# Kernel tuning notes

Measured on AMD Instinct MI355X. Metric: run time of the kernel, lower is better.

Reference implementation:

```python
import jax, jax.numpy as jnp
import numpy as np

B, N, HID, E, H = 4, 256, 256, 64, 4
OUT = HID // 2          # 128
D = OUT // H            # 32
AGG = H * (2 * D + 1)   # 260 = concat(mean D, attn_sum 1, max D) per head


def setup_inputs() -> dict:
    key = jax.random.key(0)
    ks = jax.random.split(key, 7)
    s = 0.05
    return {
        "h_x": jax.random.normal(ks[0], (B, N, HID), jnp.float32),
        "h_e": jax.random.normal(ks[1], (B, N, N, E), jnp.float32),
        "h_m": jnp.ones((B, N), jnp.float32),
        "W_Q": jax.random.normal(ks[2], (OUT, HID), jnp.float32) * s,
        "W_K": jax.random.normal(ks[3], (OUT, E), jnp.float32) * s,
        "W_V": jax.random.normal(ks[4], (OUT, E), jnp.float32) * s,
        "W_R": jax.random.normal(ks[5], (OUT, AGG), jnp.float32) * s,
    }


def reference(h_x, h_e, h_m, W_Q, W_K, W_V, W_R):
    # queries from node features: [B,H,N,D]
    h_q = (h_x @ W_Q.T).reshape(B, N, H, D).transpose(0, 2, 1, 3)
    # keys/values from dense pairwise edge features: [B,H,N,N,D]
    h_k = jnp.einsum('bnme,ce->bnmc', h_e, W_K).reshape(B, N, N, H, D).transpose(0, 3, 1, 2, 4)
    h_v = jnp.einsum('bnme,ce->bnmc', h_e, W_V).reshape(B, N, N, H, D).transpose(0, 3, 1, 2, 4)
    # broadcast dot: [B,H,N,N]
    scores = jnp.einsum('bhnd,bhnmd->bhnm', h_q, h_k) / np.float32(np.sqrt(D))
    # per-node mask broadcast as [B,1,N,1] (masks query rows)
    scores = jnp.where(h_m[:, None, :, None] == 0, -jnp.inf, scores)
    # NOTE: original code softmaxes over dim=1 = HEAD axis (faithful)
    attn = jax.nn.softmax(scores, axis=1)                      # [B,H,N,N]
    attn_w = attn[..., None] * h_v                             # [B,H,N,N,D]
    aggr_sum = attn_w.sum(axis=3)                              # [B,H,N,D]
    attn_sum = attn.sum(axis=3, keepdims=True) + 1e-8          # [B,H,N,1]
    aggr_mean = aggr_sum / attn_sum
    aggr_max = attn_w.max(axis=3)                              # [B,H,N,D]
    multi = jnp.concatenate([aggr_mean, attn_sum, aggr_max], axis=-1)  # [B,H,N,2D+1]
    aggr_out = multi.transpose(0, 2, 1, 3).reshape(B, N, AGG)  # [B,N,260]
    return aggr_out @ W_R.T                                    # [B,N,OUT]
```

## Files before the change

### kernel.cpp

```cpp
#include <hip/hip_runtime.h>
#include <hip/hip_bf16.h>

constexpr int Bb   = 4;
constexpr int Nn   = 256;
constexpr int HID  = 256;
constexpr int Ee   = 64;
constexpr int Hh   = 4;
constexpr int OUTc = 128;
constexpr int Dd   = 32;
constexpr int AGG  = 260;

typedef __attribute__((ext_vector_type(8))) short short8;
typedef __attribute__((ext_vector_type(4))) float floatx4;
typedef __attribute__((ext_vector_type(2))) float floatx2;

__device__ __forceinline__ unsigned pk2(float a, float b) {
    union { __hip_bfloat162 h; unsigned u; } cv;
    cv.h = __float22bfloat162_rn(float2{a, b});
    return cv.u;
}

__device__ __forceinline__ short8 pack8(floatx4 f0, floatx4 f1) {
    union { short8 s; unsigned u[4]; } r;
    r.u[0] = pk2(f0[0], f0[1]);
    r.u[1] = pk2(f0[2], f0[3]);
    r.u[2] = pk2(f1[0], f1[1]);
    r.u[3] = pk2(f1[2], f1[3]);
    return r.s;
}

__device__ __forceinline__ void gload16(const float* g, float* l) {
    __builtin_amdgcn_global_load_lds(
        (const __attribute__((address_space(1))) void*)g,
        (__attribute__((address_space(3))) void*)l, 16, 0, 0);
}

__global__ __launch_bounds__(256, 2)
void eama_fused(const float* __restrict__ h_x, const float* __restrict__ h_e,
                const float* __restrict__ h_m,
                const float* __restrict__ W_Q, const float* __restrict__ W_K,
                const float* __restrict__ W_V, const float* __restrict__ W_R,
                float* __restrict__ out)
{
    __shared__ __align__(16) float sStage[4][2][4][64][4];
    __shared__ __align__(16) float sS[4][16][4];
    __shared__ __align__(16) unsigned short sWin[256 * 8];
    __shared__ __align__(16) float sQp[256];

    const int tid  = threadIdx.x;
    const int lane = tid & 63;
    const int w    = tid >> 6;
    const int ncol = lane & 15;
    const int q8   = lane >> 4;
    const int bn   = blockIdx.x;
    const float maskv = h_m[bn];

    const float* heb = h_e + (size_t)bn * Nn * Ee;
    const float* arq = heb + (size_t)(w * 64 + ncol) * Ee + q8 * 8;

    #define STAGE(it_, buf_) do { \
        const float* ar_ = arq + (size_t)(it_) * 16 * Ee; \
        gload16(ar_,      &sStage[w][buf_][0][0][0]); \
        gload16(ar_ + 4,  &sStage[w][buf_][1][0][0]); \
        gload16(ar_ + 32, &sStage[w][buf_][2][0][0]); \
        gload16(ar_ + 36, &sStage[w][buf_][3][0][0]); \
    } while (0)

    STAGE(0, 0);
    STAGE(1, 1);

    short8 bfV[8][2];
    {
        const int ncol_e = tid & 15;
        const int q8_e   = (tid >> 4) & 3;
        const int ks_e   = (tid >> 6) & 1;
        const int cthi   = tid >> 7;
        #pragma unroll
        for (int c = 0; c < 4; ++c) {
            const int ct = c * 2 + cthi;
            const float* row = W_V + (size_t)(ct * 16 + ncol_e) * Ee + ks_e * 32 + q8_e * 8;
            short8 v = pack8(*(const floatx4*)row, *(const floatx4*)(row + 4));
            *(short8*)&sWin[tid * 8] = v;
            __syncthreads();
            #pragma unroll
            for (int m = 0; m < 4; ++m)
                bfV[c * 2 + (m >> 1)][m & 1] = *(const short8*)&sWin[(m * 64 + lane) * 8];
            __syncthreads();
        }
    }

    {
        const int c = tid & 127, half = tid >> 7;
        const float* wq = W_Q + (size_t)c * HID + half * 128;
        const float* xr = h_x + (size_t)bn * HID + half * 128;
        float acc = 0.f;
        #pragma unroll
        for (int i = 0; i < 32; ++i) {
            floatx4 a = *(const floatx4*)(wq + i * 4);
            floatx4 x = *(const floatx4*)(xr + i * 4);
            acc = fmaf(a[0], x[0], fmaf(a[1], x[1], fmaf(a[2], x[2], fmaf(a[3], x[3], acc))));
        }
        sQp[tid] = acc;
    }
    __syncthreads();
    if (tid < 128) sQp[tid] += sQp[tid + 128];
    __syncthreads();

    float* sU = &sS[0][0][0];
    {
        const int h = tid >> 6, e = tid & 63;
        float acc = 0.f;
        #pragma unroll
        for (int d = 0; d < 32; ++d)
            acc = fmaf(sQp[h * 32 + d], W_K[(size_t)(h * Dd + d) * Ee + e], acc);
        sU[h * 64 + e] = acc * 0.1767766952966369f;
    }
    __syncthreads();

    short8 bu0 = {0, 0, 0, 0, 0, 0, 0, 0};
    short8 bu1 = {0, 0, 0, 0, 0, 0, 0, 0};
    if (ncol < Hh) {
        bu0 = pack8(*(const floatx4*)&sU[ncol * 64 + q8 * 8],
                    *(const floatx4*)&sU[ncol * 64 + q8 * 8 + 4]);
        bu1 = pack8(*(const floatx4*)&sU[ncol * 64 + 32 + q8 * 8],
                    *(const floatx4*)&sU[ncol * 64 + 32 + q8 * 8 + 4]);
    }
    __syncthreads();

    float vs[8], vm[8], asumH = 0.f;
    #pragma unroll
    for (int ct = 0; ct < 8; ++ct) { vs[ct] = 0.f; vm[ct] = -3.402823466e38f; }

    #pragma unroll
    for (int it = 0; it < 4; ++it) {
        const int buf = it & 1;
        if (it < 3) asm volatile("s_waitcnt vmcnt(4)" ::: "memory");
        else        asm volatile("s_waitcnt vmcnt(0)" ::: "memory");

        floatx4 c0 = *(const floatx4*)&sStage[w][buf][0][lane][0];
        floatx4 c1 = *(const floatx4*)&sStage[w][buf][1][lane][0];
        floatx4 c2 = *(const floatx4*)&sStage[w][buf][2][lane][0];
        floatx4 c3 = *(const floatx4*)&sStage[w][buf][3][lane][0];
        short8 af0 = pack8(c0, c1);
        short8 af1 = pack8(c2, c3);
        if (it < 2) {
            asm volatile("s_waitcnt lgkmcnt(0)" ::: "memory");
            STAGE(it + 2, buf);
        }

        floatx4 accV[8], accS = (floatx4){0, 0, 0, 0};
        #pragma unroll
        for (int ct = 0; ct < 8; ++ct) accV[ct] = (floatx4){0, 0, 0, 0};
        #pragma unroll
        for (int ct = 0; ct < 8; ++ct) {
            accV[ct] = __builtin_amdgcn_mfma_f32_16x16x32_bf16(af0, bfV[ct][0], accV[ct], 0, 0, 0);
            accV[ct] = __builtin_amdgcn_mfma_f32_16x16x32_bf16(af1, bfV[ct][1], accV[ct], 0, 0, 0);
        }
        accS = __builtin_amdgcn_mfma_f32_16x16x32_bf16(af0, bu0, accS, 0, 0, 0);
        accS = __builtin_amdgcn_mfma_f32_16x16x32_bf16(af1, bu1, accS, 0, 0, 0);

        if (ncol < Hh) {
            #pragma unroll
            for (int r = 0; r < 4; ++r)
                sS[w][q8 * 4 + r][ncol] = (maskv != 0.f) ? accS[r] : -1e30f;
        }
        __builtin_amdgcn_wave_barrier();

        #pragma unroll
        for (int r = 0; r < 4; ++r) {
            floatx4 sc = *(const floatx4*)&sS[w][q8 * 4 + r][0];
            float e0 = __expf(sc[0]), e1 = __expf(sc[1]);
            float e2 = __expf(sc[2]), e3 = __expf(sc[3]);
            float inv = 1.f / ((e0 + e1) + (e2 + e3));
            float a0 = e0 * inv, a1 = e1 * inv, a2 = e2 * inv, a3 = e3 * inv;
            asumH += (ncol & 2) ? ((ncol & 1) ? a3 : a2) : ((ncol & 1) ? a1 : a0);
            float p;
            p = a0 * accV[0][r]; vs[0] += p; vm[0] = fmaxf(vm[0], p);
            p = a0 * accV[1][r]; vs[1] += p; vm[1] = fmaxf(vm[1], p);
            p = a1 * accV[2][r]; vs[2] += p; vm[2] = fmaxf(vm[2], p);
            p = a1 * accV[3][r]; vs[3] += p; vm[3] = fmaxf(vm[3], p);
            p = a2 * accV[4][r]; vs[4] += p; vm[4] = fmaxf(vm[4], p);
            p = a2 * accV[5][r]; vs[5] += p; vm[5] = fmaxf(vm[5], p);
            p = a3 * accV[6][r]; vs[6] += p; vm[6] = fmaxf(vm[6], p);
            p = a3 * accV[7][r]; vs[7] += p; vm[7] = fmaxf(vm[7], p);
        }
        __builtin_amdgcn_wave_barrier();
    }
    #undef STAGE

    #pragma unroll
    for (int ct = 0; ct < 8; ++ct) {
        vs[ct] += __shfl_xor(vs[ct], 16, 64);
        vs[ct] += __shfl_xor(vs[ct], 32, 64);
        vm[ct] = fmaxf(vm[ct], __shfl_xor(vm[ct], 16, 64));
        vm[ct] = fmaxf(vm[ct], __shfl_xor(vm[ct], 32, 64));
    }
    asumH += __shfl_xor(asumH, 16, 64);
    asumH += __shfl_xor(asumH, 32, 64);

    float* SB = &sStage[0][0][0][0][0];
    if (lane < 16) {
        #pragma unroll
        for (int ct = 0; ct < 8; ++ct) {
            SB[w * 2048 + ct * 16 + lane]       = vs[ct];
            SB[w * 2048 + 128 + ct * 16 + lane] = vm[ct];
        }
    }
    if (lane < Hh) SB[w * 2048 + 256 + lane] = asumH;
    __syncthreads();
    if (tid < Hh) {
        SB[512 + tid] = 1e-8f +
            (SB[0 * 2048 + 256 + tid] + SB[1 * 2048 + 256 + tid]) +
            (SB[2 * 2048 + 256 + tid] + SB[3 * 2048 + 256 + tid]);
    }
    __syncthreads();
    if (tid < OUTc) {
        float vsum = (SB[0 * 2048 + tid] + SB[1 * 2048 + tid]) +
                     (SB[2 * 2048 + tid] + SB[3 * 2048 + tid]);
        float vmax = fmaxf(fmaxf(SB[0 * 2048 + 128 + tid], SB[1 * 2048 + 128 + tid]),
                           fmaxf(SB[2 * 2048 + 128 + tid], SB[3 * 2048 + 128 + tid]));
        const int h = tid >> 5, d = tid & 31;
        SB[768 + h * 65 + d]      = vsum / SB[512 + h];
        SB[768 + h * 65 + 33 + d] = vmax;
        if (tid < Hh) SB[768 + tid * 65 + 32] = SB[512 + tid];
    }
    __syncthreads();
    {
        const int c = tid & 127, part = tid >> 7;
        const int j0 = part * 130;
        const float* wr = W_R + (size_t)c * AGG + j0;
        const float* sM = SB + 768;
        float a0 = 0.f, a1 = 0.f, a2 = 0.f, a3 = 0.f;
        #pragma unroll 8
        for (int j = 0; j < 128; j += 4) {
            floatx2 A  = *(const floatx2*)(wr + j);
            floatx2 Bv = *(const floatx2*)(wr + j + 2);
            a0 = fmaf(sM[j0 + j],     A[0],  a0);
            a1 = fmaf(sM[j0 + j + 1], A[1],  a1);
            a2 = fmaf(sM[j0 + j + 2], Bv[0], a2);
            a3 = fmaf(sM[j0 + j + 3], Bv[1], a3);
        }
        floatx2 T = *(const floatx2*)(wr + 128);
        a0 = fmaf(sM[j0 + 128], T[0], a0);
        a1 = fmaf(sM[j0 + 129], T[1], a1);
        SB[1100 + part * 128 + c] = (a0 + a1) + (a2 + a3);
    }
    __syncthreads();
    if (tid < OUTc)
        out[(size_t)bn * OUTc + tid] = SB[1100 + tid] + SB[1100 + 128 + tid];
}

extern "C" void kernel_launch(void* const* d_in, const int* in_sizes, int n_in,
                              void* d_out, int out_size, void* d_ws, size_t ws_size,
                              hipStream_t stream) {
    const float* h_x = (const float*)d_in[0];
    const float* h_e = (const float*)d_in[1];
    const float* h_m = (const float*)d_in[2];
    const float* W_Q = (const float*)d_in[3];
    const float* W_K = (const float*)d_in[4];
    const float* W_V = (const float*)d_in[5];
    const float* W_R = (const float*)d_in[6];
    float* out = (float*)d_out;

    eama_fused<<<dim3(Bb * Nn), dim3(256), 0, stream>>>(
        h_x, h_e, h_m, W_Q, W_K, W_V, W_R, out);
}
```

Baseline: 141.2 us.

## Stage full h_e slice to LDS after prologue instead of double-buffered prefetch

Replaces the two-deep double-buffered h_e prefetch, which was issued before the W_V/Q/U prologue, with a four-deep buffer that holds the block's whole h_e slice. All four stages are now issued after the prologue, and each iteration waits on a decreasing vmcnt. The W_V bf16 fragment conversion is reorganized to use a larger LDS scratch with two barrier rounds instead of four. The mask check is moved into an opaque register value. The change doubles LDS usage, which may reduce occupancy, and it no longer overlaps the h_e loads with the prologue.

Measured after the change: 142.3 us. No clear change (+0.8%).

```diff
diff --git a/kernel.cpp b/kernel.cpp
--- a/kernel.cpp
+++ b/kernel.cpp
@@ -42,9 +42,9 @@
                 const float* __restrict__ W_V, const float* __restrict__ W_R,
                 float* __restrict__ out)
 {
-    __shared__ __align__(16) float sStage[4][2][4][64][4];
+    __shared__ __align__(16) float sStage[4][4][4][64][4];
     __shared__ __align__(16) float sS[4][16][4];
-    __shared__ __align__(16) unsigned short sWin[256 * 8];
+    __shared__ __align__(16) unsigned short sWin[512 * 8];
     __shared__ __align__(16) float sQp[256];
 
     const int tid  = threadIdx.x;
@@ -53,40 +53,29 @@
     const int ncol = lane & 15;
     const int q8   = lane >> 4;
     const int bn   = blockIdx.x;
-    const float maskv = h_m[bn];
-
-    const float* heb = h_e + (size_t)bn * Nn * Ee;
-    const float* arq = heb + (size_t)(w * 64 + ncol) * Ee + q8 * 8;
-
-    #define STAGE(it_, buf_) do { \
-        const float* ar_ = arq + (size_t)(it_) * 16 * Ee; \
-        gload16(ar_,      &sStage[w][buf_][0][0][0]); \
-        gload16(ar_ + 4,  &sStage[w][buf_][1][0][0]); \
-        gload16(ar_ + 32, &sStage[w][buf_][2][0][0]); \
-        gload16(ar_ + 36, &sStage[w][buf_][3][0][0]); \
-    } while (0)
-
-    STAGE(0, 0);
-    STAGE(1, 1);
+
+    int moki = (h_m[bn] != 0.f) ? 1 : 0;
+    asm volatile("" : "+v"(moki));
 
     short8 bfV[8][2];
-    {
-        const int ncol_e = tid & 15;
-        const int q8_e   = (tid >> 4) & 3;
-        const int ks_e   = (tid >> 6) & 1;
-        const int cthi   = tid >> 7;
-        #pragma unroll
-        for (int c = 0; c < 4; ++c) {
-            const int ct = c * 2 + cthi;
-            const float* row = W_V + (size_t)(ct * 16 + ncol_e) * Ee + ks_e * 32 + q8_e * 8;
-            short8 v = pack8(*(const floatx4*)row, *(const floatx4*)(row + 4));
-            *(short8*)&sWin[tid * 8] = v;
-            __syncthreads();
+    #pragma unroll
+    for (int c = 0; c < 2; ++c) {
+        #pragma unroll
+        for (int kk = 0; kk < 2; ++kk) {
+            const int k  = kk * 256 + tid;
+            const int ct = c * 4 + (k >> 7);
+            const float* src = W_V + (size_t)(ct * 16 + (k & 15)) * Ee
+                             + ((k >> 6) & 1) * 32 + ((k >> 4) & 3) * 8;
+            *(short8*)&sWin[(size_t)k * 8] = pack8(*(const floatx4*)src,
+                                                   *(const floatx4*)(src + 4));
+        }
+        __syncthreads();
+        #pragma unroll
+        for (int ct4 = 0; ct4 < 4; ++ct4)
             #pragma unroll
-            for (int m = 0; m < 4; ++m)
-                bfV[c * 2 + (m >> 1)][m & 1] = *(const short8*)&sWin[(m * 64 + lane) * 8];
-            __syncthreads();
-        }
+            for (int ks = 0; ks < 2; ++ks)
+                bfV[c * 4 + ct4][ks] = *(const short8*)&sWin[((ct4 * 2 + ks) * 64 + lane) * 8];
+        __syncthreads();
     }
 
     {
@@ -127,26 +116,38 @@
     }
     __syncthreads();
 
+    __builtin_amdgcn_sched_barrier(0);
+    {
+        const float* heb = h_e + (size_t)bn * Nn * Ee;
+        const float* arq = heb + (size_t)(w * 64 + ncol) * Ee + q8 * 8;
+        #pragma unroll
+        for (int it = 0; it < 4; ++it) {
+            const float* ar = arq + (size_t)it * 16 * Ee;
+            gload16(ar,      &sStage[w][it][0][0][0]);
+            gload16(ar + 4,  &sStage[w][it][1][0][0]);
+            gload16(ar + 32, &sStage[w][it][2][0][0]);
+            gload16(ar + 36, &sStage[w][it][3][0][0]);
+        }
+    }
+    __builtin_amdgcn_sched_barrier(0);
+
     float vs[8], vm[8], asumH = 0.f;
     #pragma unroll
     for (int ct = 0; ct < 8; ++ct) { vs[ct] = 0.f; vm[ct] = -3.402823466e38f; }
 
     #pragma unroll
     for (int it = 0; it < 4; ++it) {
-        const int buf = it & 1;
-        if (it < 3) asm volatile("s_waitcnt vmcnt(4)" ::: "memory");
-        else        asm volatile("s_waitcnt vmcnt(0)" ::: "memory");
-
-        floatx4 c0 = *(const floatx4*)&sStage[w][buf][0][lane][0];
-        floatx4 c1 = *(const floatx4*)&sStage[w][buf][1][lane][0];
-        floatx4 c2 = *(const floatx4*)&sStage[w][buf][2][lane][0];
-        floatx4 c3 = *(const floatx4*)&sStage[w][buf][3][lane][0];
+        if (it == 0)      asm volatile("s_waitcnt vmcnt(12)" ::: "memory");
+        else if (it == 1) asm volatile("s_waitcnt vmcnt(8)"  ::: "memory");
+        else if (it == 2) asm volatile("s_waitcnt vmcnt(4)"  ::: "memory");
+        else              asm volatile("s_waitcnt vmcnt(0)"  ::: "memory");
+
+        floatx4 c0 = *(const floatx4*)&sStage[w][it][0][lane][0];
+        floatx4 c1 = *(const floatx4*)&sStage[w][it][1][lane][0];
+        floatx4 c2 = *(const floatx4*)&sStage[w][it][2][lane][0];
+        floatx4 c3 = *(const floatx4*)&sStage[w][it][3][lane][0];
         short8 af0 = pack8(c0, c1);
         short8 af1 = pack8(c2, c3);
-        if (it < 2) {
-            asm volatile("s_waitcnt lgkmcnt(0)" ::: "memory");
-            STAGE(it + 2, buf);
-        }
 
         floatx4 accV[8], accS = (floatx4){0, 0, 0, 0};
         #pragma unroll
@@ -162,7 +163,7 @@
         if (ncol < Hh) {
             #pragma unroll
             for (int r = 0; r < 4; ++r)
-                sS[w][q8 * 4 + r][ncol] = (maskv != 0.f) ? accS[r] : -1e30f;
+                sS[w][q8 * 4 + r][ncol] = moki ? accS[r] : -1e30f;
         }
         __builtin_amdgcn_wave_barrier();
 
@@ -186,7 +187,6 @@
         }
         __builtin_amdgcn_wave_barrier();
     }
-    #undef STAGE
 
     #pragma unroll
     for (int ct = 0; ct < 8; ++ct) {
@@ -202,23 +202,23 @@
     if (lane < 16) {
         #pragma unroll
         for (int ct = 0; ct < 8; ++ct) {
-            SB[w * 2048 + ct * 16 + lane]       = vs[ct];
-            SB[w * 2048 + 128 + ct * 16 + lane] = vm[ct];
-        }
-    }
-    if (lane < Hh) SB[w * 2048 + 256 + lane] = asumH;
+            SB[w * 4096 + ct * 16 + lane]       = vs[ct];
+            SB[w * 4096 + 128 + ct * 16 + lane] = vm[ct];
+        }
+    }
+    if (lane < Hh) SB[w * 4096 + 256 + lane] = asumH;
     __syncthreads();
     if (tid < Hh) {
         SB[512 + tid] = 1e-8f +
-            (SB[0 * 2048 + 256 + tid] + SB[1 * 2048 + 256 + tid]) +
-            (SB[2 * 2048 + 256 + tid] + SB[3 * 2048 + 256 + tid]);
+            (SB[0 * 4096 + 256 + tid] + SB[1 * 4096 + 256 + tid]) +
+            (SB[2 * 4096 + 256 + tid] + SB[3 * 4096 + 256 + tid]);
     }
     __syncthreads();
     if (tid < OUTc) {
-        float vsum = (SB[0 * 2048 + tid] + SB[1 * 2048 + tid]) +
-                     (SB[2 * 2048 + tid] + SB[3 * 2048 + tid]);
-        float vmax = fmaxf(fmaxf(SB[0 * 2048 + 128 + tid], SB[1 * 2048 + 128 + tid]),
-                           fmaxf(SB[2 * 2048 + 128 + tid], SB[3 * 2048 + 128 + tid]));
+        float vsum = (SB[0 * 4096 + tid] + SB[1 * 4096 + tid]) +
+                     (SB[2 * 4096 + tid] + SB[3 * 4096 + tid]);
+        float vmax = fmaxf(fmaxf(SB[0 * 4096 + 128 + tid], SB[1 * 4096 + 128 + tid]),
+                           fmaxf(SB[2 * 4096 + 128 + tid], SB[3 * 4096 + 128 + tid]));
         const int h = tid >> 5, d = tid & 31;
         SB[768 + h * 65 + d]      = vsum / SB[512 + h];
         SB[768 + h * 65 + 33 + d] = vmax;
```
